# Kernel optimization log

Measured on AMD Instinct MI355X. Metric: run time of the kernel, lower is better.

## Reference

```python
import jax, jax.numpy as jnp
import numpy as np

N_BLADES = 8
D_BLADE = 128
D_FFN = 512
LN_EPS = 1e-5


def _build_cayley_signs():
    """Cl(3,0) Cayley table: blades indexed by bitmask over {e1,e2,e3}.
    signs[i, j, k] = s where blade_i * blade_j = s * blade_k (Euclidean metric)."""
    def reorder_sign(a, b):
        a >>= 1
        total = 0
        while a:
            total += bin(a & b).count('1')
            a >>= 1
        return 1.0 if total % 2 == 0 else -1.0
    signs = np.zeros((8, 8, 8), dtype=np.float32)
    for i in range(8):
        for j in range(8):
            signs[i, j, i ^ j] = reorder_sign(i, j)
    return jnp.asarray(signs)


def setup_inputs() -> dict:
    key = jax.random.key(0)
    k_x, k_g, k_u, k_d = jax.random.split(key, 4)
    B, T = 4, 4096
    x = jax.random.normal(k_x, (B, T, N_BLADES, D_BLADE), dtype=jnp.float32)
    return {
        'x': x,
        'interaction_weights': jnp.full((N_BLADES, N_BLADES), 0.1, dtype=jnp.float32),
        'geo_gate': jnp.asarray(0.5, dtype=jnp.float32),
        'ln_w': jnp.ones((D_BLADE,), dtype=jnp.float32),
        'ln_b': jnp.zeros((D_BLADE,), dtype=jnp.float32),
        'w_gate': jax.random.normal(k_g, (D_FFN, D_BLADE), dtype=jnp.float32) * 0.02,
        'w_up': jax.random.normal(k_u, (D_FFN, D_BLADE), dtype=jnp.float32) * 0.02,
        'w_down': jax.random.normal(k_d, (D_BLADE, D_FFN), dtype=jnp.float32) * 0.02,
        'cayley_signs': _build_cayley_signs(),
    }


def reference(x, interaction_weights, geo_gate, ln_w, ln_b, w_gate, w_up, w_down, cayley_signs):
    # --- full geometric self-product via Cayley table ---
    w = jax.nn.sigmoid(interaction_weights)              # (i, j)
    signed = cayley_signs * w[:, :, None]                # (i, j, k): fold weights into sign tensor
    # result[b,t,k,d] = sum_ij signed[i,j,k] * x[b,t,i,d] * x[b,t,j,d]
    geo = jnp.einsum('btid,btjd,ijk->btkd', x, x, signed)
    # --- residual gate between geometric product and input ---
    gate = jax.nn.sigmoid(geo_gate)
    mixed = gate * geo + (1.0 - gate) * x                # (B, T, N, D)
    # --- per-blade LayerNorm over d_blade ---
    mu = jnp.mean(mixed, axis=-1, keepdims=True)
    var = jnp.mean(jnp.square(mixed - mu), axis=-1, keepdims=True)
    normed = (mixed - mu) * jax.lax.rsqrt(var + LN_EPS) * ln_w + ln_b
    # --- SwiGLU FFN (no biases) ---
    g = jnp.einsum('btnd,fd->btnf', normed, w_gate)
    u = jnp.einsum('btnd,fd->btnf', normed, w_up)
    h = jax.nn.silu(g) * u
    out = jnp.einsum('btnf,df->btnd', h, w_down)
    return x + out
```

## Files before the change

### kernel.cpp

```cpp
#include <hip/hip_runtime.h>
#include <hip/hip_bf16.h>

typedef unsigned short ushort_t;
typedef __bf16 bf16_t;
typedef bf16_t bf16x8 __attribute__((ext_vector_type(8)));
typedef unsigned short u16x8v __attribute__((ext_vector_type(8)));
typedef float f32x4 __attribute__((ext_vector_type(4)));

#define D 128
#define NB 8
#define DFFN 512
#define TPB 16
#define MROWS 128
#define FCH 64
#define NCH 8
#define LN_EPS 1e-5f

__device__ __forceinline__ ushort_t bf16_rne(float f) {
  union { float f; unsigned u; } c; c.f = f;
  unsigned u = c.u;
  unsigned r = (u + 0x7FFFu + ((u >> 16) & 1u)) >> 16;
  return (ushort_t)r;
}

__device__ __forceinline__ bf16x8 loadfrag_bf(const ushort_t* p) {
  u16x8v v = *(const u16x8v*)p;
  return __builtin_bit_cast(bf16x8, v);
}

__device__ __forceinline__ bf16x8 load8_cvt(const float* p) {
  f32x4 a = *(const f32x4*)p;
  f32x4 b = *(const f32x4*)(p + 4);
  u16x8v r;
  r[0] = bf16_rne(a[0]); r[1] = bf16_rne(a[1]);
  r[2] = bf16_rne(a[2]); r[3] = bf16_rne(a[3]);
  r[4] = bf16_rne(b[0]); r[5] = bf16_rne(b[1]);
  r[6] = bf16_rne(b[2]); r[7] = bf16_rne(b[3]);
  return __builtin_bit_cast(bf16x8, r);
}

__device__ __forceinline__ f32x4 mfma16(bf16x8 a, bf16x8 b, f32x4 c) {
  return __builtin_amdgcn_mfma_f32_16x16x32_bf16(a, b, c, 0, 0, 0);
}

__global__ void cvt_weights(const float* __restrict__ wg,
                            const float* __restrict__ wu,
                            const float* __restrict__ wd,
                            ushort_t* __restrict__ o) {
  int i = blockIdx.x * 256 + threadIdx.x;
  const int n1 = DFFN * D;
  float v;
  if (i < n1)            v = wg[i];
  else if (i < 2 * n1)   v = wu[i - n1];
  else                   v = wd[i - 2 * n1];
  o[i] = bf16_rne(v);
}

template <bool WS_BF16>
__global__ __launch_bounds__(256, 2)
void fused_geo_ffn(const float* __restrict__ x,
                   const float* __restrict__ iw,
                   const float* __restrict__ geo_gate,
                   const float* __restrict__ ln_w,
                   const float* __restrict__ ln_b,
                   const float* __restrict__ w_gate_f,
                   const float* __restrict__ w_up_f,
                   const float* __restrict__ w_down_f,
                   const float* __restrict__ cayley,
                   const ushort_t* __restrict__ wg_bf,
                   const ushort_t* __restrict__ wu_bf,
                   const ushort_t* __restrict__ wd_bf,
                   float* __restrict__ out) {
  __shared__ float sg[64];
  __shared__ ushort_t A_lds[MROWS * 128];
  __shared__ ushort_t H_lds[MROWS * FCH];

  const int tid = threadIdx.x;
  const int w = tid >> 6;
  const int l = tid & 63;
  const int lg = l >> 4;
  const int ln16 = l & 15;
  const int kbase = lg * 8;

  if (tid < 64) {
    int i = tid >> 3, j = tid & 7;
    float s = cayley[(i * 8 + j) * 8 + (i ^ j)];
    float wv = iw[i * 8 + j];
    sg[tid] = s / (1.0f + __expf(-wv));
  }
  __syncthreads();

  float sgr[64];
#pragma unroll
  for (int t = 0; t < 64; ++t) sgr[t] = sg[t];

  const float gate = 1.0f / (1.0f + __expf(-geo_gate[0]));
  const float2 lw = *(const float2*)(ln_w + 2 * l);
  const float2 lb = *(const float2*)(ln_b + 2 * l);

  const long tok0 = (long)blockIdx.x * TPB;

  for (int tt = 0; tt < 4; ++tt) {
    int ltok = w * 4 + tt;
    const float* xp = x + (tok0 + ltok) * (long)(NB * D);
    float2 xv[8];
#pragma unroll
    for (int i = 0; i < 8; ++i) xv[i] = *(const float2*)(xp + i * D + 2 * l);
#pragma unroll
    for (int k = 0; k < 8; ++k) {
      float2 g; g.x = 0.f; g.y = 0.f;
#pragma unroll
      for (int i = 0; i < 8; ++i) {
        float s = sgr[i * 8 + (i ^ k)];
        g.x += s * xv[i].x * xv[i ^ k].x;
        g.y += s * xv[i].y * xv[i ^ k].y;
      }
      float2 m;
      m.x = gate * g.x + (1.0f - gate) * xv[k].x;
      m.y = gate * g.y + (1.0f - gate) * xv[k].y;
      float s1 = m.x + m.y;
      float s2 = m.x * m.x + m.y * m.y;
#pragma unroll
      for (int off = 32; off; off >>= 1) {
        s1 += __shfl_xor(s1, off, 64);
        s2 += __shfl_xor(s2, off, 64);
      }
      float mu = s1 * (1.0f / 128.0f);
      float var = s2 * (1.0f / 128.0f) - mu * mu;
      float rs = rsqrtf(var + LN_EPS);
      float nx = (m.x - mu) * rs * lw.x + lb.x;
      float ny = (m.y - mu) * rs * lw.y + lb.y;
      int row = ltok * 8 + k;
      int col = (2 * l) ^ ((row & 7) << 3);
      unsigned pack = (unsigned)bf16_rne(nx) | ((unsigned)bf16_rne(ny) << 16);
      *(unsigned*)&A_lds[row * 128 + col] = pack;
    }
  }
  __syncthreads();

  f32x4 oacc[8][2];
#pragma unroll
  for (int mt = 0; mt < 8; ++mt)
#pragma unroll
    for (int nt = 0; nt < 2; ++nt)
#pragma unroll
      for (int r = 0; r < 4; ++r) oacc[mt][nt][r] = 0.f;

  for (int ch = 0; ch < NCH; ++ch) {
    f32x4 gacc[8], uacc[8];
#pragma unroll
    for (int mt = 0; mt < 8; ++mt)
#pragma unroll
      for (int r = 0; r < 4; ++r) { gacc[mt][r] = 0.f; uacc[mt][r] = 0.f; }

    const int fbase = ch * FCH + w * 16 + ln16;
    bf16x8 bg[4], bu[4];
#pragma unroll
    for (int ks = 0; ks < 4; ++ks) {
      int koff = ks * 32 + kbase;
      if (WS_BF16) {
        bg[ks] = loadfrag_bf(wg_bf + fbase * 128 + koff);
        bu[ks] = loadfrag_bf(wu_bf + fbase * 128 + koff);
      } else {
        bg[ks] = load8_cvt(w_gate_f + fbase * 128 + koff);
        bu[ks] = load8_cvt(w_up_f + fbase * 128 + koff);
      }
    }
#pragma unroll
    for (int mt = 0; mt < 8; ++mt) {
#pragma unroll
      for (int ks = 0; ks < 4; ++ks) {
        int row = mt * 16 + ln16;
        int col = (ks * 32 + kbase) ^ ((row & 7) << 3);
        bf16x8 a = *(const bf16x8*)&A_lds[row * 128 + col];
        gacc[mt] = mfma16(a, bg[ks], gacc[mt]);
        uacc[mt] = mfma16(a, bu[ks], uacc[mt]);
      }
    }
#pragma unroll
    for (int mt = 0; mt < 8; ++mt) {
#pragma unroll
      for (int r = 0; r < 4; ++r) {
        float gv = gacc[mt][r], uv = uacc[mt][r];
        float hv = gv / (1.0f + __expf(-gv)) * uv;
        int row = mt * 16 + lg * 4 + r;
        int col = (w * 16 + ln16) ^ ((row & 7) << 3);
        H_lds[row * FCH + col] = bf16_rne(hv);
      }
    }
    __syncthreads();
    bf16x8 b2[2][2];
#pragma unroll
    for (int nt = 0; nt < 2; ++nt) {
      int dcol = w * 32 + nt * 16 + ln16;
#pragma unroll
      for (int ks = 0; ks < 2; ++ks) {
        int foff = ch * FCH + ks * 32 + kbase;
        if (WS_BF16) b2[nt][ks] = loadfrag_bf(wd_bf + dcol * DFFN + foff);
        else         b2[nt][ks] = load8_cvt(w_down_f + dcol * DFFN + foff);
      }
    }
#pragma unroll
    for (int mt = 0; mt < 8; ++mt) {
#pragma unroll
      for (int ks = 0; ks < 2; ++ks) {
        int row = mt * 16 + ln16;
        int col = (ks * 32 + kbase) ^ ((row & 7) << 3);
        bf16x8 a2 = *(const bf16x8*)&H_lds[row * FCH + col];
        oacc[mt][0] = mfma16(a2, b2[0][ks], oacc[mt][0]);
        oacc[mt][1] = mfma16(a2, b2[1][ks], oacc[mt][1]);
      }
    }
    __syncthreads();
  }

#pragma unroll
  for (int mt = 0; mt < 8; ++mt) {
#pragma unroll
    for (int nt = 0; nt < 2; ++nt) {
#pragma unroll
      for (int r = 0; r < 4; ++r) {
        long row = tok0 * NB + mt * 16 + lg * 4 + r;
        int d = w * 32 + nt * 16 + ln16;
        long idx = row * D + d;
        out[idx] = x[idx] + oacc[mt][nt][r];
      }
    }
  }
}

extern "C" void kernel_launch(void* const* d_in, const int* in_sizes, int n_in,
                              void* d_out, int out_size, void* d_ws, size_t ws_size,
                              hipStream_t stream) {
  const float* x   = (const float*)d_in[0];
  const float* iw  = (const float*)d_in[1];
  const float* gg  = (const float*)d_in[2];
  const float* lnw = (const float*)d_in[3];
  const float* lnb = (const float*)d_in[4];
  const float* wg  = (const float*)d_in[5];
  const float* wu  = (const float*)d_in[6];
  const float* wd  = (const float*)d_in[7];
  const float* cs  = (const float*)d_in[8];
  float* out = (float*)d_out;

  int ntok = in_sizes[0] / (NB * D);
  int nblk = ntok / TPB;

  const int wtot = 3 * DFFN * D;
  bool use_ws = ws_size >= (size_t)wtot * sizeof(ushort_t);
  if (use_ws) {
    ushort_t* wbf = (ushort_t*)d_ws;
    cvt_weights<<<wtot / 256, 256, 0, stream>>>(wg, wu, wd, wbf);
    fused_geo_ffn<true><<<nblk, 256, 0, stream>>>(
        x, iw, gg, lnw, lnb, wg, wu, wd, cs,
        wbf, wbf + DFFN * D, wbf + 2 * DFFN * D, out);
  } else {
    fused_geo_ffn<false><<<nblk, 256, 0, stream>>>(
        x, iw, gg, lnw, lnb, wg, wu, wd, cs,
        (const ushort_t*)nullptr, (const ushort_t*)nullptr, (const ushort_t*)nullptr, out);
  }
}
```

Measured before the change: 123.4 us.

## Give each wave its own 32-row FFN tile and drop block-level barriers

```diff
diff --git a/kernel.cpp b/kernel.cpp
--- a/kernel.cpp
+++ b/kernel.cpp
@@ -6,14 +6,12 @@
 typedef bf16_t bf16x8 __attribute__((ext_vector_type(8)));
 typedef unsigned short u16x8v __attribute__((ext_vector_type(8)));
 typedef float f32x4 __attribute__((ext_vector_type(4)));
+typedef unsigned uint32x2 __attribute__((ext_vector_type(2)));
 
 #define D 128
 #define NB 8
 #define DFFN 512
 #define TPB 16
-#define MROWS 128
-#define FCH 64
-#define NCH 8
 #define LN_EPS 1e-5f
 
 __device__ __forceinline__ ushort_t bf16_rne(float f) {
@@ -21,6 +19,12 @@
   unsigned u = c.u;
   unsigned r = (u + 0x7FFFu + ((u >> 16) & 1u)) >> 16;
   return (ushort_t)r;
+}
+
+__device__ __forceinline__ unsigned cvt_pk_bf16(float lo, float hi) {
+  unsigned r;
+  asm("v_cvt_pk_bf16_f32 %0, %1, %2" : "=v"(r) : "v"(lo), "v"(hi));
+  return r;
 }
 
 __device__ __forceinline__ bf16x8 loadfrag_bf(const ushort_t* p) {
@@ -41,6 +45,10 @@
 
 __device__ __forceinline__ f32x4 mfma16(bf16x8 a, bf16x8 b, f32x4 c) {
   return __builtin_amdgcn_mfma_f32_16x16x32_bf16(a, b, c, 0, 0, 0);
+}
+
+__device__ __forceinline__ float readlane_f(float v, int lane) {
+  return __builtin_bit_cast(float, __builtin_amdgcn_readlane(__builtin_bit_cast(int, v), lane));
 }
 
 __global__ void cvt_weights(const float* __restrict__ wg,
@@ -57,7 +65,7 @@
 }
 
 template <bool WS_BF16>
-__global__ __launch_bounds__(256, 2)
+__global__ __launch_bounds__(256, 3)
 void fused_geo_ffn(const float* __restrict__ x,
                    const float* __restrict__ iw,
                    const float* __restrict__ geo_gate,
@@ -71,159 +79,197 @@
                    const ushort_t* __restrict__ wu_bf,
                    const ushort_t* __restrict__ wd_bf,
                    float* __restrict__ out) {
-  __shared__ float sg[64];
-  __shared__ ushort_t A_lds[MROWS * 128];
-  __shared__ ushort_t H_lds[MROWS * FCH];
+  __shared__ ushort_t A_lds[4][32 * 128];
+  __shared__ ushort_t H_lds[4][32 * 32];
 
   const int tid = threadIdx.x;
   const int w = tid >> 6;
   const int l = tid & 63;
   const int lg = l >> 4;
   const int ln16 = l & 15;
-  const int kbase = lg * 8;
-
-  if (tid < 64) {
-    int i = tid >> 3, j = tid & 7;
-    float s = cayley[(i * 8 + j) * 8 + (i ^ j)];
-    float wv = iw[i * 8 + j];
-    sg[tid] = s / (1.0f + __expf(-wv));
-  }
-  __syncthreads();
-
-  float sgr[64];
-#pragma unroll
-  for (int t = 0; t < 64; ++t) sgr[t] = sg[t];
+
+  ushort_t* A = &A_lds[w][0];
+  ushort_t* Hl = &H_lds[w][0];
+
+  float sgv;
+  {
+    int i_l = l >> 3, j_l = l & 7;
+    float s = cayley[(i_l * 8 + j_l) * 8 + (i_l ^ j_l)];
+    sgv = s / (1.0f + __expf(-iw[i_l * 8 + j_l]));
+  }
+  float cd[8];
+  float cp[28];
+#pragma unroll
+  for (int i = 0; i < 8; ++i) cd[i] = readlane_f(sgv, i * 8 + i);
+  {
+    int p = 0;
+#pragma unroll
+    for (int i = 0; i < 8; ++i)
+#pragma unroll
+      for (int j = i + 1; j < 8; ++j) {
+        cp[p] = readlane_f(sgv, i * 8 + j) + readlane_f(sgv, j * 8 + i);
+        ++p;
+      }
+  }
 
   const float gate = 1.0f / (1.0f + __expf(-geo_gate[0]));
-  const float2 lw = *(const float2*)(ln_w + 2 * l);
-  const float2 lb = *(const float2*)(ln_b + 2 * l);
+  const float ogate = 1.0f - gate;
+  const float2 lwv = *(const float2*)(ln_w + 2 * l);
+  const float2 lbv = *(const float2*)(ln_b + 2 * l);
 
   const long tok0 = (long)blockIdx.x * TPB;
 
   for (int tt = 0; tt < 4; ++tt) {
-    int ltok = w * 4 + tt;
-    const float* xp = x + (tok0 + ltok) * (long)(NB * D);
+    const float* xp = x + (tok0 + w * 4 + tt) * (long)(NB * D);
     float2 xv[8];
 #pragma unroll
     for (int i = 0; i < 8; ++i) xv[i] = *(const float2*)(xp + i * D + 2 * l);
+    float2 geo[8];
+#pragma unroll
+    for (int k = 0; k < 8; ++k) { geo[k].x = 0.f; geo[k].y = 0.f; }
+#pragma unroll
+    for (int i = 0; i < 8; ++i) {
+      geo[0].x += cd[i] * xv[i].x * xv[i].x;
+      geo[0].y += cd[i] * xv[i].y * xv[i].y;
+    }
+    {
+      int p = 0;
+#pragma unroll
+      for (int i = 0; i < 8; ++i)
+#pragma unroll
+        for (int j = i + 1; j < 8; ++j) {
+          int k = i ^ j;
+          geo[k].x += cp[p] * (xv[i].x * xv[j].x);
+          geo[k].y += cp[p] * (xv[i].y * xv[j].y);
+          ++p;
+        }
+    }
+    int rowb = tt * 8;
 #pragma unroll
     for (int k = 0; k < 8; ++k) {
-      float2 g; g.x = 0.f; g.y = 0.f;
-#pragma unroll
-      for (int i = 0; i < 8; ++i) {
-        float s = sgr[i * 8 + (i ^ k)];
-        g.x += s * xv[i].x * xv[i ^ k].x;
-        g.y += s * xv[i].y * xv[i ^ k].y;
-      }
-      float2 m;
-      m.x = gate * g.x + (1.0f - gate) * xv[k].x;
-      m.y = gate * g.y + (1.0f - gate) * xv[k].y;
-      float s1 = m.x + m.y;
-      float s2 = m.x * m.x + m.y * m.y;
+      float mx = gate * geo[k].x + ogate * xv[k].x;
+      float my = gate * geo[k].y + ogate * xv[k].y;
+      float s1 = mx + my;
+      float s2 = mx * mx + my * my;
 #pragma unroll
       for (int off = 32; off; off >>= 1) {
         s1 += __shfl_xor(s1, off, 64);
         s2 += __shfl_xor(s2, off, 64);
       }
       float mu = s1 * (1.0f / 128.0f);
-      float var = s2 * (1.0f / 128.0f) - mu * mu;
-      float rs = rsqrtf(var + LN_EPS);
-      float nx = (m.x - mu) * rs * lw.x + lb.x;
-      float ny = (m.y - mu) * rs * lw.y + lb.y;
-      int row = ltok * 8 + k;
-      int col = (2 * l) ^ ((row & 7) << 3);
-      unsigned pack = (unsigned)bf16_rne(nx) | ((unsigned)bf16_rne(ny) << 16);
-      *(unsigned*)&A_lds[row * 128 + col] = pack;
-    }
-  }
-  __syncthreads();
-
-  f32x4 oacc[8][2];
-#pragma unroll
-  for (int mt = 0; mt < 8; ++mt)
-#pragma unroll
-    for (int nt = 0; nt < 2; ++nt)
+      float rs = rsqrtf(s2 * (1.0f / 128.0f) - mu * mu + LN_EPS);
+      float nx = (mx - mu) * rs * lwv.x + lbv.x;
+      float ny = (my - mu) * rs * lwv.y + lbv.y;
+      int row = rowb + k;
+      int colb = (4 * l) ^ ((row & 7) << 4);
+      *(unsigned*)((char*)A + row * 256 + colb) = cvt_pk_bf16(nx, ny);
+    }
+  }
+
+  bf16x8 af[2][4];
+#pragma unroll
+  for (int mt = 0; mt < 2; ++mt) {
+    int row = mt * 16 + ln16;
+#pragma unroll
+    for (int ks = 0; ks < 4; ++ks) {
+      int u = (ks * 4 + lg) ^ (row & 7);
+      af[mt][ks] = *(const bf16x8*)((const char*)A + row * 256 + u * 16);
+    }
+  }
+
+  f32x4 oacc[2][8];
+#pragma unroll
+  for (int mt = 0; mt < 2; ++mt)
+#pragma unroll
+    for (int nt = 0; nt < 8; ++nt)
 #pragma unroll
       for (int r = 0; r < 4; ++r) oacc[mt][nt][r] = 0.f;
 
-  for (int ch = 0; ch < NCH; ++ch) {
-    f32x4 gacc[8], uacc[8];
-#pragma unroll
-    for (int mt = 0; mt < 8; ++mt)
-#pragma unroll
-      for (int r = 0; r < 4; ++r) { gacc[mt][r] = 0.f; uacc[mt][r] = 0.f; }
-
-    const int fbase = ch * FCH + w * 16 + ln16;
-    bf16x8 bg[4], bu[4];
-#pragma unroll
-    for (int ks = 0; ks < 4; ++ks) {
-      int koff = ks * 32 + kbase;
-      if (WS_BF16) {
-        bg[ks] = loadfrag_bf(wg_bf + fbase * 128 + koff);
-        bu[ks] = loadfrag_bf(wu_bf + fbase * 128 + koff);
-      } else {
-        bg[ks] = load8_cvt(w_gate_f + fbase * 128 + koff);
-        bu[ks] = load8_cvt(w_up_f + fbase * 128 + koff);
-      }
-    }
-#pragma unroll
-    for (int mt = 0; mt < 8; ++mt) {
+  const int hrow = ln16;
+  const int hsw0 = (ln16 >> 1) & 3;
+
+  for (int ch = 0; ch < 16; ++ch) {
+    const int f0 = ch * 32;
+
+    bf16x8 bd[8];
+#pragma unroll
+    for (int nt = 0; nt < 8; ++nt) {
+      int dcol = nt * 16 + ln16;
+      if (WS_BF16) bd[nt] = loadfrag_bf(wd_bf + dcol * DFFN + f0 + lg * 8);
+      else         bd[nt] = load8_cvt(w_down_f + dcol * DFFN + f0 + lg * 8);
+    }
+
+    f32x4 gt[2][2], ut[2][2];
+#pragma unroll
+    for (int ft = 0; ft < 2; ++ft)
+#pragma unroll
+      for (int mt = 0; mt < 2; ++mt)
+#pragma unroll
+        for (int r = 0; r < 4; ++r) { gt[ft][mt][r] = 0.f; ut[ft][mt][r] = 0.f; }
+
+#pragma unroll
+    for (int ft = 0; ft < 2; ++ft) {
+      int frow = f0 + ft * 16 + ln16;
 #pragma unroll
       for (int ks = 0; ks < 4; ++ks) {
-        int row = mt * 16 + ln16;
-        int col = (ks * 32 + kbase) ^ ((row & 7) << 3);
-        bf16x8 a = *(const bf16x8*)&A_lds[row * 128 + col];
-        gacc[mt] = mfma16(a, bg[ks], gacc[mt]);
-        uacc[mt] = mfma16(a, bu[ks], uacc[mt]);
-      }
-    }
-#pragma unroll
-    for (int mt = 0; mt < 8; ++mt) {
-#pragma unroll
-      for (int r = 0; r < 4; ++r) {
-        float gv = gacc[mt][r], uv = uacc[mt][r];
-        float hv = gv / (1.0f + __expf(-gv)) * uv;
-        int row = mt * 16 + lg * 4 + r;
-        int col = (w * 16 + ln16) ^ ((row & 7) << 3);
-        H_lds[row * FCH + col] = bf16_rne(hv);
-      }
-    }
-    __syncthreads();
-    bf16x8 b2[2][2];
-#pragma unroll
-    for (int nt = 0; nt < 2; ++nt) {
-      int dcol = w * 32 + nt * 16 + ln16;
-#pragma unroll
-      for (int ks = 0; ks < 2; ++ks) {
-        int foff = ch * FCH + ks * 32 + kbase;
-        if (WS_BF16) b2[nt][ks] = loadfrag_bf(wd_bf + dcol * DFFN + foff);
-        else         b2[nt][ks] = load8_cvt(w_down_f + dcol * DFFN + foff);
-      }
-    }
-#pragma unroll
-    for (int mt = 0; mt < 8; ++mt) {
-#pragma unroll
-      for (int ks = 0; ks < 2; ++ks) {
-        int row = mt * 16 + ln16;
-        int col = (ks * 32 + kbase) ^ ((row & 7) << 3);
-        bf16x8 a2 = *(const bf16x8*)&H_lds[row * FCH + col];
-        oacc[mt][0] = mfma16(a2, b2[0][ks], oacc[mt][0]);
-        oacc[mt][1] = mfma16(a2, b2[1][ks], oacc[mt][1]);
-      }
-    }
-    __syncthreads();
-  }
-
-#pragma unroll
-  for (int mt = 0; mt < 8; ++mt) {
-#pragma unroll
-    for (int nt = 0; nt < 2; ++nt) {
-#pragma unroll
-      for (int r = 0; r < 4; ++r) {
-        long row = tok0 * NB + mt * 16 + lg * 4 + r;
-        int d = w * 32 + nt * 16 + ln16;
-        long idx = row * D + d;
-        out[idx] = x[idx] + oacc[mt][nt][r];
+        bf16x8 bg, bu;
+        if (WS_BF16) {
+          bg = loadfrag_bf(wg_bf + frow * D + ks * 32 + lg * 8);
+          bu = loadfrag_bf(wu_bf + frow * D + ks * 32 + lg * 8);
+        } else {
+          bg = load8_cvt(w_gate_f + frow * D + ks * 32 + lg * 8);
+          bu = load8_cvt(w_up_f + frow * D + ks * 32 + lg * 8);
+        }
+        gt[ft][0] = mfma16(bg, af[0][ks], gt[ft][0]);
+        gt[ft][1] = mfma16(bg, af[1][ks], gt[ft][1]);
+        ut[ft][0] = mfma16(bu, af[0][ks], ut[ft][0]);
+        ut[ft][1] = mfma16(bu, af[1][ks], ut[ft][1]);
+      }
+    }
+
+#pragma unroll
+    for (int mt = 0; mt < 2; ++mt) {
+      int m = mt * 16 + hrow;
+#pragma unroll
+      for (int ft = 0; ft < 2; ++ft) {
+        float h[4];
+#pragma unroll
+        for (int r = 0; r < 4; ++r) {
+          float gv = gt[ft][mt][r], uv = ut[ft][mt][r];
+          h[r] = gv / (1.0f + __expf(-gv)) * uv;
+        }
+        uint32x2 pk;
+        pk[0] = cvt_pk_bf16(h[0], h[1]);
+        pk[1] = cvt_pk_bf16(h[2], h[3]);
+        int u16i = (ft * 2 + (lg >> 1)) ^ hsw0;
+        char* p = (char*)Hl + m * 64 + u16i * 16 + (lg & 1) * 8;
+        *(uint32x2*)p = pk;
+      }
+    }
+
+#pragma unroll
+    for (int mt = 0; mt < 2; ++mt) {
+      int m = mt * 16 + ln16;
+      int u = lg ^ hsw0;
+      bf16x8 ha = *(const bf16x8*)((const char*)Hl + m * 64 + u * 16);
+#pragma unroll
+      for (int nt = 0; nt < 8; ++nt)
+        oacc[mt][nt] = mfma16(ha, bd[nt], oacc[mt][nt]);
+    }
+  }
+
+  const long rowg0 = tok0 * NB + (long)w * 32;
+#pragma unroll
+  for (int mt = 0; mt < 2; ++mt) {
+#pragma unroll
+    for (int r = 0; r < 4; ++r) {
+      long row = rowg0 + mt * 16 + lg * 4 + r;
+      const float* xp = x + row * D;
+      float* op = out + row * D;
+#pragma unroll
+      for (int nt = 0; nt < 8; ++nt) {
+        int d = nt * 16 + ln16;
+        op[d] = xp[d] + oacc[mt][nt][r];
       }
     }
   }
```

Result: slower. 210.7 us (+70.8%).

## Split fused kernel into geo+LayerNorm and FFN MFMA kernels via bf16 workspace

Applied to the files above, without the earlier changes.

```diff
diff --git a/kernel.cpp b/kernel.cpp
--- a/kernel.cpp
+++ b/kernel.cpp
@@ -6,14 +6,12 @@
 typedef bf16_t bf16x8 __attribute__((ext_vector_type(8)));
 typedef unsigned short u16x8v __attribute__((ext_vector_type(8)));
 typedef float f32x4 __attribute__((ext_vector_type(4)));
+typedef unsigned uint32x2 __attribute__((ext_vector_type(2)));
+typedef unsigned uint32x4 __attribute__((ext_vector_type(4)));
 
 #define D 128
 #define NB 8
 #define DFFN 512
-#define TPB 16
-#define MROWS 128
-#define FCH 64
-#define NCH 8
 #define LN_EPS 1e-5f
 
 __device__ __forceinline__ ushort_t bf16_rne(float f) {
@@ -21,6 +19,12 @@
   unsigned u = c.u;
   unsigned r = (u + 0x7FFFu + ((u >> 16) & 1u)) >> 16;
   return (ushort_t)r;
+}
+
+__device__ __forceinline__ unsigned cvt_pk_bf16(float lo, float hi) {
+  unsigned r;
+  asm("v_cvt_pk_bf16_f32 %0, %1, %2" : "=v"(r) : "v"(lo), "v"(hi));
+  return r;
 }
 
 __device__ __forceinline__ bf16x8 loadfrag_bf(const ushort_t* p) {
@@ -41,6 +45,16 @@
 
 __device__ __forceinline__ f32x4 mfma16(bf16x8 a, bf16x8 b, f32x4 c) {
   return __builtin_amdgcn_mfma_f32_16x16x32_bf16(a, b, c, 0, 0, 0);
+}
+
+__device__ __forceinline__ float readlane_f(float v, int lane) {
+  return __builtin_bit_cast(float, __builtin_amdgcn_readlane(__builtin_bit_cast(int, v), lane));
+}
+
+typedef const __attribute__((address_space(1))) void gv_t;
+typedef __attribute__((address_space(3))) void lv_t;
+__device__ __forceinline__ void gload_lds16(const void* g, void* l) {
+  __builtin_amdgcn_global_load_lds((gv_t*)g, (lv_t*)l, 16, 0, 0);
 }
 
 __global__ void cvt_weights(const float* __restrict__ wg,
@@ -54,6 +68,210 @@
   else if (i < 2 * n1)   v = wu[i - n1];
   else                   v = wd[i - 2 * n1];
   o[i] = bf16_rne(v);
+}
+
+__global__ __launch_bounds__(256)
+void geo_ln(const float* __restrict__ x,
+            const float* __restrict__ iw,
+            const float* __restrict__ geo_gate,
+            const float* __restrict__ ln_w,
+            const float* __restrict__ ln_b,
+            const float* __restrict__ cayley,
+            ushort_t* __restrict__ Aout) {
+  const int tid = threadIdx.x;
+  const int w = tid >> 6;
+  const int l = tid & 63;
+  const int g = l >> 4;
+  const int q = l & 15;
+
+  float sgv;
+  {
+    int i_l = l >> 3, j_l = l & 7;
+    float s = cayley[(i_l * 8 + j_l) * 8 + (i_l ^ j_l)];
+    sgv = s / (1.0f + __expf(-iw[i_l * 8 + j_l]));
+  }
+  float cd[8], cp[28];
+#pragma unroll
+  for (int i = 0; i < 8; ++i) cd[i] = readlane_f(sgv, i * 8 + i);
+  {
+    int p = 0;
+#pragma unroll
+    for (int i = 0; i < 8; ++i)
+#pragma unroll
+      for (int j = i + 1; j < 8; ++j) { cp[p] = readlane_f(sgv, i * 8 + j) + readlane_f(sgv, j * 8 + i); ++p; }
+  }
+  const float gate = 1.0f / (1.0f + __expf(-geo_gate[0]));
+  const float ogate = 1.0f - gate;
+
+  const f32x4 lw0 = *(const f32x4*)(ln_w + q * 8);
+  const f32x4 lw1 = *(const f32x4*)(ln_w + q * 8 + 4);
+  const f32x4 lb0 = *(const f32x4*)(ln_b + q * 8);
+  const f32x4 lb1 = *(const f32x4*)(ln_b + q * 8 + 4);
+
+  const long tok = (long)blockIdx.x * 16 + w * 4 + g;
+  const float* xp = x + tok * (NB * D) + q * 8;
+
+  f32x4 xa[8], xb[8];
+#pragma unroll
+  for (int i = 0; i < 8; ++i) { xa[i] = *(const f32x4*)(xp + i * D); xb[i] = *(const f32x4*)(xp + i * D + 4); }
+
+  f32x4 ga[8], gb[8];
+#pragma unroll
+  for (int k = 0; k < 8; ++k) { ga[k] = 0.f; gb[k] = 0.f; }
+#pragma unroll
+  for (int i = 0; i < 8; ++i) {
+    ga[0] += cd[i] * (xa[i] * xa[i]);
+    gb[0] += cd[i] * (xb[i] * xb[i]);
+  }
+  {
+    int p = 0;
+#pragma unroll
+    for (int i = 0; i < 8; ++i)
+#pragma unroll
+      for (int j = i + 1; j < 8; ++j) {
+        int k = i ^ j;
+        ga[k] += cp[p] * (xa[i] * xa[j]);
+        gb[k] += cp[p] * (xb[i] * xb[j]);
+        ++p;
+      }
+  }
+
+  ushort_t* Arow0 = Aout + tok * (8 * D);
+#pragma unroll
+  for (int k = 0; k < 8; ++k) {
+    f32x4 m0 = gate * ga[k] + ogate * xa[k];
+    f32x4 m1 = gate * gb[k] + ogate * xb[k];
+    float s1 = (m0[0] + m0[1]) + (m0[2] + m0[3]) + (m1[0] + m1[1]) + (m1[2] + m1[3]);
+    float s2 = m0[0]*m0[0] + m0[1]*m0[1] + m0[2]*m0[2] + m0[3]*m0[3]
+             + m1[0]*m1[0] + m1[1]*m1[1] + m1[2]*m1[2] + m1[3]*m1[3];
+#pragma unroll
+    for (int off = 8; off; off >>= 1) {
+      s1 += __shfl_xor(s1, off, 64);
+      s2 += __shfl_xor(s2, off, 64);
+    }
+    float mu = s1 * (1.0f / 128.0f);
+    float rs = rsqrtf(s2 * (1.0f / 128.0f) - mu * mu + LN_EPS);
+    float nb2 = -mu * rs;
+    f32x4 n0, n1;
+#pragma unroll
+    for (int e = 0; e < 4; ++e) {
+      n0[e] = (m0[e] * rs + nb2) * lw0[e] + lb0[e];
+      n1[e] = (m1[e] * rs + nb2) * lw1[e] + lb1[e];
+    }
+    uint32x4 pk;
+    pk[0] = cvt_pk_bf16(n0[0], n0[1]);
+    pk[1] = cvt_pk_bf16(n0[2], n0[3]);
+    pk[2] = cvt_pk_bf16(n1[0], n1[1]);
+    pk[3] = cvt_pk_bf16(n1[2], n1[3]);
+    *(uint32x4*)(Arow0 + k * D + ((q ^ k) * 8)) = pk;
+  }
+}
+
+__global__ __launch_bounds__(256, 3)
+void ffn_mfma(const ushort_t* __restrict__ Abf,
+              const float* __restrict__ x,
+              const ushort_t* __restrict__ wg_bf,
+              const ushort_t* __restrict__ wu_bf,
+              const ushort_t* __restrict__ wd_bf,
+              float* __restrict__ out) {
+  __shared__ ushort_t A[128 * 128];
+  __shared__ ushort_t H[128 * 64];
+
+  const int tid = threadIdx.x;
+  const int w = tid >> 6;
+  const int l = tid & 63;
+  const int lg = l >> 4;
+  const int ln16 = l & 15;
+
+  const long row0 = (long)blockIdx.x * 128;
+
+  {
+    const ushort_t* src = Abf + row0 * D;
+#pragma unroll
+    for (int i = 0; i < 8; ++i) {
+      int seg = w * 8 + i;
+      gload_lds16(src + seg * 512 + l * 8, &A[seg * 512]);
+    }
+  }
+  __syncthreads();
+
+  f32x4 oacc[8][2];
+#pragma unroll
+  for (int mt = 0; mt < 8; ++mt)
+#pragma unroll
+    for (int nt = 0; nt < 2; ++nt)
+#pragma unroll
+      for (int r = 0; r < 4; ++r) oacc[mt][nt][r] = 0.f;
+
+  for (int ch = 0; ch < 8; ++ch) {
+    const int fbase = ch * 64 + w * 16 + ln16;
+    bf16x8 bg[4], bu[4], bd[2][2];
+#pragma unroll
+    for (int ks = 0; ks < 4; ++ks) {
+      bg[ks] = loadfrag_bf(wg_bf + fbase * D + ks * 32 + lg * 8);
+      bu[ks] = loadfrag_bf(wu_bf + fbase * D + ks * 32 + lg * 8);
+    }
+#pragma unroll
+    for (int nt = 0; nt < 2; ++nt) {
+      int dcol = w * 32 + nt * 16 + ln16;
+#pragma unroll
+      for (int ks = 0; ks < 2; ++ks)
+        bd[nt][ks] = loadfrag_bf(wd_bf + dcol * DFFN + ch * 64 + ks * 32 + lg * 8);
+    }
+
+#pragma unroll
+    for (int mt = 0; mt < 8; ++mt) {
+      const int row = mt * 16 + ln16;
+      f32x4 gacc = 0.f, uacc = 0.f;
+#pragma unroll
+      for (int ks = 0; ks < 4; ++ks) {
+        int unit = (ks * 4 + lg) ^ (row & 7);
+        bf16x8 a = *(const bf16x8*)&A[row * D + unit * 8];
+        gacc = mfma16(bg[ks], a, gacc);
+        uacc = mfma16(bu[ks], a, uacc);
+      }
+      float h[4];
+#pragma unroll
+      for (int r = 0; r < 4; ++r) {
+        float gv = gacc[r], uv = uacc[r];
+        h[r] = gv / (1.0f + __expf(-gv)) * uv;
+      }
+      uint32x2 pk;
+      pk[0] = cvt_pk_bf16(h[0], h[1]);
+      pk[1] = cvt_pk_bf16(h[2], h[3]);
+      int u = (w * 2 + (lg >> 1)) ^ (row & 7);
+      *(uint32x2*)&H[row * 64 + u * 8 + (lg & 1) * 4] = pk;
+    }
+    __syncthreads();
+
+#pragma unroll
+    for (int mt = 0; mt < 8; ++mt) {
+      const int row = mt * 16 + ln16;
+#pragma unroll
+      for (int ks = 0; ks < 2; ++ks) {
+        int u = (ks * 4 + lg) ^ (row & 7);
+        bf16x8 hfrag = *(const bf16x8*)&H[row * 64 + u * 8];
+        oacc[mt][0] = mfma16(hfrag, bd[0][ks], oacc[mt][0]);
+        oacc[mt][1] = mfma16(hfrag, bd[1][ks], oacc[mt][1]);
+      }
+    }
+    __syncthreads();
+  }
+
+#pragma unroll
+  for (int mt = 0; mt < 8; ++mt) {
+#pragma unroll
+    for (int r = 0; r < 4; ++r) {
+      long rowg = row0 + mt * 16 + lg * 4 + r;
+      const float* xp = x + rowg * D;
+      float* op = out + rowg * D;
+#pragma unroll
+      for (int nt = 0; nt < 2; ++nt) {
+        int d = w * 32 + nt * 16 + ln16;
+        op[d] = xp[d] + oacc[mt][nt][r];
+      }
+    }
+  }
 }
 
 template <bool WS_BF16>
@@ -72,8 +290,8 @@
                    const ushort_t* __restrict__ wd_bf,
                    float* __restrict__ out) {
   __shared__ float sg[64];
-  __shared__ ushort_t A_lds[MROWS * 128];
-  __shared__ ushort_t H_lds[MROWS * FCH];
+  __shared__ ushort_t A_lds[128 * 128];
+  __shared__ ushort_t H_lds[128 * 64];
 
   const int tid = threadIdx.x;
   const int w = tid >> 6;
@@ -85,11 +303,9 @@
   if (tid < 64) {
     int i = tid >> 3, j = tid & 7;
     float s = cayley[(i * 8 + j) * 8 + (i ^ j)];
-    float wv = iw[i * 8 + j];
-    sg[tid] = s / (1.0f + __expf(-wv));
+    sg[tid] = s / (1.0f + __expf(-iw[i * 8 + j]));
   }
   __syncthreads();
-
   float sgr[64];
 #pragma unroll
   for (int t = 0; t < 64; ++t) sgr[t] = sg[t];
@@ -97,8 +313,7 @@
   const float gate = 1.0f / (1.0f + __expf(-geo_gate[0]));
   const float2 lw = *(const float2*)(ln_w + 2 * l);
   const float2 lb = *(const float2*)(ln_b + 2 * l);
-
-  const long tok0 = (long)blockIdx.x * TPB;
+  const long tok0 = (long)blockIdx.x * 16;
 
   for (int tt = 0; tt < 4; ++tt) {
     int ltok = w * 4 + tt;
@@ -126,14 +341,12 @@
         s2 += __shfl_xor(s2, off, 64);
       }
       float mu = s1 * (1.0f / 128.0f);
-      float var = s2 * (1.0f / 128.0f) - mu * mu;
-      float rs = rsqrtf(var + LN_EPS);
+      float rs = rsqrtf(s2 * (1.0f / 128.0f) - mu * mu + LN_EPS);
       float nx = (m.x - mu) * rs * lw.x + lb.x;
       float ny = (m.y - mu) * rs * lw.y + lb.y;
       int row = ltok * 8 + k;
-      int col = (2 * l) ^ ((row & 7) << 3);
-      unsigned pack = (unsigned)bf16_rne(nx) | ((unsigned)bf16_rne(ny) << 16);
-      *(unsigned*)&A_lds[row * 128 + col] = pack;
+      int colb = (4 * l) ^ ((row & 7) << 4);
+      *(unsigned*)((char*)A_lds + row * 256 + colb) = cvt_pk_bf16(nx, ny);
     }
   }
   __syncthreads();
@@ -146,84 +359,80 @@
 #pragma unroll
       for (int r = 0; r < 4; ++r) oacc[mt][nt][r] = 0.f;
 
-  for (int ch = 0; ch < NCH; ++ch) {
-    f32x4 gacc[8], uacc[8];
-#pragma unroll
-    for (int mt = 0; mt < 8; ++mt)
-#pragma unroll
-      for (int r = 0; r < 4; ++r) { gacc[mt][r] = 0.f; uacc[mt][r] = 0.f; }
-
-    const int fbase = ch * FCH + w * 16 + ln16;
+  for (int ch = 0; ch < 8; ++ch) {
+    const int fbase = ch * 64 + w * 16 + ln16;
     bf16x8 bg[4], bu[4];
 #pragma unroll
     for (int ks = 0; ks < 4; ++ks) {
       int koff = ks * 32 + kbase;
       if (WS_BF16) {
-        bg[ks] = loadfrag_bf(wg_bf + fbase * 128 + koff);
-        bu[ks] = loadfrag_bf(wu_bf + fbase * 128 + koff);
+        bg[ks] = loadfrag_bf(wg_bf + fbase * D + koff);
+        bu[ks] = loadfrag_bf(wu_bf + fbase * D + koff);
       } else {
-        bg[ks] = load8_cvt(w_gate_f + fbase * 128 + koff);
-        bu[ks] = load8_cvt(w_up_f + fbase * 128 + koff);
+        bg[ks] = load8_cvt(w_gate_f + fbase * D + koff);
+        bu[ks] = load8_cvt(w_up_f + fbase * D + koff);
       }
     }
 #pragma unroll
     for (int mt = 0; mt < 8; ++mt) {
+      const int row = mt * 16 + ln16;
+      f32x4 gacc = 0.f, uacc = 0.f;
 #pragma unroll
       for (int ks = 0; ks < 4; ++ks) {
-        int row = mt * 16 + ln16;
-        int col = (ks * 32 + kbase) ^ ((row & 7) << 3);
-        bf16x8 a = *(const bf16x8*)&A_lds[row * 128 + col];
-        gacc[mt] = mfma16(a, bg[ks], gacc[mt]);
-        uacc[mt] = mfma16(a, bu[ks], uacc[mt]);
-      }
-    }
+        int colb = ((ks * 32 + kbase) * 2) ^ ((row & 7) << 4);
+        bf16x8 a = *(const bf16x8*)((const char*)A_lds + row * 256 + colb);
+        gacc = mfma16(bg[ks], a, gacc);
+        uacc = mfma16(bu[ks], a, uacc);
+      }
+      float h[4];
+#pragma unroll
+      for (int r = 0; r < 4; ++r) {
+        float gv = gacc[r], uv = uacc[r];
+        h[r] = gv / (1.0f + __expf(-gv)) * uv;
+      }
+      uint32x2 pk;
+      pk[0] = cvt_pk_bf16(h[0], h[1]);
+      pk[1] = cvt_pk_bf16(h[2], h[3]);
+      int u = (w * 2 + (lg >> 1)) ^ (row & 7);
+      *(uint32x2*)&H_lds[row * 64 + u * 8 + (lg & 1) * 4] = pk;
+    }
+    __syncthreads();
 #pragma unroll
     for (int mt = 0; mt < 8; ++mt) {
-#pragma unroll
-      for (int r = 0; r < 4; ++r) {
-        float gv = gacc[mt][r], uv = uacc[mt][r];
-        float hv = gv / (1.0f + __expf(-gv)) * uv;
-        int row = mt * 16 + lg * 4 + r;
-        int col = (w * 16 + ln16) ^ ((row & 7) << 3);
-        H_lds[row * FCH + col] = bf16_rne(hv);
+      const int row = mt * 16 + ln16;
+#pragma unroll
+      for (int ks = 0; ks < 2; ++ks) {
+        int u = (ks * 4 + lg) ^ (row & 7);
+        bf16x8 hfrag = *(const bf16x8*)&H_lds[row * 64 + u * 8];
+        bf16x8 b0, b1;
+        int dcol0 = w * 32 + ln16;
+        int foff = ch * 64 + ks * 32 + kbase;
+        if (WS_BF16) {
+          b0 = loadfrag_bf(wd_bf + dcol0 * DFFN + foff);
+          b1 = loadfrag_bf(wd_bf + (dcol0 + 16) * DFFN + foff);
+        } else {
+          b0 = load8_cvt(w_down_f + dcol0 * DFFN + foff);
+          b1 = load8_cvt(w_down_f + (dcol0 + 16) * DFFN + foff);
+        }
+        oacc[mt][0] = mfma16(hfrag, b0, oacc[mt][0]);
+        oacc[mt][1] = mfma16(hfrag, b1, oacc[mt][1]);
       }
     }
     __syncthreads();
-    bf16x8 b2[2][2];
-#pragma unroll
-    for (int nt = 0; nt < 2; ++nt) {
-      int dcol = w * 32 + nt * 16 + ln16;
-#pragma unroll
-      for (int ks = 0; ks < 2; ++ks) {
-        int foff = ch * FCH + ks * 32 + kbase;
-        if (WS_BF16) b2[nt][ks] = loadfrag_bf(wd_bf + dcol * DFFN + foff);
-        else         b2[nt][ks] = load8_cvt(w_down_f + dcol * DFFN + foff);
-      }
-    }
-#pragma unroll
-    for (int mt = 0; mt < 8; ++mt) {
-#pragma unroll
-      for (int ks = 0; ks < 2; ++ks) {
-        int row = mt * 16 + ln16;
-        int col = (ks * 32 + kbase) ^ ((row & 7) << 3);
-        bf16x8 a2 = *(const bf16x8*)&H_lds[row * FCH + col];
-        oacc[mt][0] = mfma16(a2, b2[0][ks], oacc[mt][0]);
-        oacc[mt][1] = mfma16(a2, b2[1][ks], oacc[mt][1]);
-      }
-    }
-    __syncthreads();
-  }
-
+  }
+
+  const long rowg0 = tok0 * NB;
 #pragma unroll
   for (int mt = 0; mt < 8; ++mt) {
 #pragma unroll
-    for (int nt = 0; nt < 2; ++nt) {
-#pragma unroll
-      for (int r = 0; r < 4; ++r) {
-        long row = tok0 * NB + mt * 16 + lg * 4 + r;
+    for (int r = 0; r < 4; ++r) {
+      long row = rowg0 + mt * 16 + lg * 4 + r;
+      const float* xp = x + row * D;
+      float* op = out + row * D;
+#pragma unroll
+      for (int nt = 0; nt < 2; ++nt) {
         int d = w * 32 + nt * 16 + ln16;
-        long idx = row * D + d;
-        out[idx] = x[idx] + oacc[mt][nt][r];
+        op[d] = xp[d] + oacc[mt][nt][r];
       }
     }
   }
@@ -243,19 +452,26 @@
   const float* cs  = (const float*)d_in[8];
   float* out = (float*)d_out;
 
-  int ntok = in_sizes[0] / (NB * D);
-  int nblk = ntok / TPB;
-
+  const int ntok = in_sizes[0] / (NB * D);
   const int wtot = 3 * DFFN * D;
-  bool use_ws = ws_size >= (size_t)wtot * sizeof(ushort_t);
-  if (use_ws) {
+  const size_t wbytes = (size_t)wtot * 2;
+  const size_t abytes = (size_t)ntok * NB * D * 2;
+
+  if (ws_size >= wbytes + abytes) {
+    ushort_t* wbf = (ushort_t*)d_ws;
+    ushort_t* act = wbf + wtot;
+    cvt_weights<<<wtot / 256, 256, 0, stream>>>(wg, wu, wd, wbf);
+    geo_ln<<<ntok / 16, 256, 0, stream>>>(x, iw, gg, lnw, lnb, cs, act);
+    ffn_mfma<<<(ntok * NB) / 128, 256, 0, stream>>>(
+        act, x, wbf, wbf + DFFN * D, wbf + 2 * DFFN * D, out);
+  } else if (ws_size >= wbytes) {
     ushort_t* wbf = (ushort_t*)d_ws;
     cvt_weights<<<wtot / 256, 256, 0, stream>>>(wg, wu, wd, wbf);
-    fused_geo_ffn<true><<<nblk, 256, 0, stream>>>(
+    fused_geo_ffn<true><<<ntok / 16, 256, 0, stream>>>(
         x, iw, gg, lnw, lnb, wg, wu, wd, cs,
         wbf, wbf + DFFN * D, wbf + 2 * DFFN * D, out);
   } else {
-    fused_geo_ffn<false><<<nblk, 256, 0, stream>>>(
+    fused_geo_ffn<false><<<ntok / 16, 256, 0, stream>>>(
         x, iw, gg, lnw, lnb, wg, wu, wd, cs,
         (const ushort_t*)nullptr, (const ushort_t*)nullptr, (const ushort_t*)nullptr, out);
   }
```

After: 149.1 us. 20.9% more time.
